# Kernel optimization log

Measured on AMD Instinct MI355X. Metric: run time of the kernel, lower is better.

## Reference

```python
import jax, jax.numpy as jnp
import numpy as np

B, N_RX, IMG_H, IMG_W = 128, 34, 512, 512
N_CAT = 5  # num_rx_categories + 1


def setup_inputs() -> dict:
    key = jax.random.key(0)
    k_pow, k_xy, k_cat, k_dw, k_db, k_cw, k_cb = jax.random.split(key, 7)
    # x_vecs columns: [power, x_coord, y_coord, category]
    powers = jax.random.normal(k_pow, (B, N_RX, 1), dtype=jnp.float32)
    coords = jax.random.randint(k_xy, (B, N_RX, 2), 0, IMG_W).astype(jnp.float32)
    cats = jax.random.randint(k_cat, (B, N_RX, 1), 0, N_CAT).astype(jnp.float32)
    x_vecs = jnp.concatenate([powers, coords, cats], axis=-1)  # [B, N_RX, 4]
    # learned per-device and per-category affine parameters (init: ones/zeros,
    # perturbed slightly so the test is non-trivial)
    device_weights = 1.0 + 0.1 * jax.random.normal(k_dw, (N_RX,), dtype=jnp.float32)
    device_bias = 0.1 * jax.random.normal(k_db, (N_RX,), dtype=jnp.float32)
    category_weights = 1.0 + 0.1 * jax.random.normal(k_cw, (N_CAT,), dtype=jnp.float32)
    category_bias = 0.1 * jax.random.normal(k_cb, (N_CAT,), dtype=jnp.float32)
    return {
        "x_vecs": x_vecs,
        "device_weights": device_weights,
        "device_bias": device_bias,
        "category_weights": category_weights,
        "category_bias": category_bias,
    }


def reference(x_vecs, device_weights, device_bias, category_weights, category_bias):
    batch, n_rx = x_vecs.shape[0], x_vecs.shape[1]
    raw_powers = x_vecs[:, :, 0]                      # [B, N]
    power_mask = (raw_powers != 0).astype(x_vecs.dtype)
    # per-device affine (device_multiplication)
    p = raw_powers * device_weights + power_mask * device_bias
    # per-category affine (category_multiplication)
    cat = x_vecs[:, :, -1].astype(jnp.int32)          # [B, N]
    p = p * category_weights[cat] + power_mask * category_bias[cat]
    # coordinate-based scatter into image grid
    coords = jnp.round(x_vecs[:, :, 1:3]).astype(jnp.int32)  # [B, N, 2] (x, y)
    b_idx = jnp.repeat(jnp.arange(batch), n_rx)
    yy = coords[:, :, 1].ravel()
    xx = coords[:, :, 0].ravel()
    x_img = jnp.zeros((batch, 2, IMG_H, IMG_W), dtype=x_vecs.dtype)
    x_img = x_img.at[b_idx, 0, yy, xx].set(p.ravel())
    x_img = x_img.at[b_idx, 1, yy, xx].set(raw_powers.ravel())
    return x_img
```

## Files before the change

kernel.cpp:

```cpp
#include <hip/hip_runtime.h>

#define B_BATCH 128
#define N_RX 34
#define IMG 512
#define N_CAT 5

__global__ void Vec2Im_scatter_kernel(const float* __restrict__ x_vecs,
                                      const float* __restrict__ device_weights,
                                      const float* __restrict__ device_bias,
                                      const float* __restrict__ category_weights,
                                      const float* __restrict__ category_bias,
                                      float* __restrict__ out) {
    int b = blockIdx.x * blockDim.x + threadIdx.x;
    if (b >= B_BATCH) return;

    const float4* xv = reinterpret_cast<const float4*>(x_vecs) + (size_t)b * N_RX;
    float* plane0 = out + (size_t)b * 2 * IMG * IMG;
    float* plane1 = plane0 + (size_t)IMG * IMG;

    for (int r = 0; r < N_RX; ++r) {
        float4 v = xv[r];
        float raw = v.x;
        float mask = (raw != 0.0f) ? 1.0f : 0.0f;
        float p = raw * device_weights[r] + mask * device_bias[r];
        int cat = (int)v.w;
        p = p * category_weights[cat] + mask * category_bias[cat];
        int xx = (int)rintf(v.y);
        int yy = (int)rintf(v.z);
        int off = yy * IMG + xx;
        plane0[off] = p;
        plane1[off] = raw;
    }
}

extern "C" void kernel_launch(void* const* d_in, const int* in_sizes, int n_in,
                              void* d_out, int out_size, void* d_ws, size_t ws_size,
                              hipStream_t stream) {
    const float* x_vecs           = (const float*)d_in[0];
    const float* device_weights   = (const float*)d_in[1];
    const float* device_bias      = (const float*)d_in[2];
    const float* category_weights = (const float*)d_in[3];
    const float* category_bias    = (const float*)d_in[4];
    float* out = (float*)d_out;

    hipMemsetAsync(d_out, 0, (size_t)out_size * sizeof(float), stream);

    Vec2Im_scatter_kernel<<<1, 128, 0, stream>>>(
        x_vecs, device_weights, device_bias, category_weights, category_bias, out);
}
```

Measured before the change: 275.7 us.

## Fuse zero-fill and scatter into one tiled nontemporal write kernel

Replaces the separate memset plus single-block scatter with one kernel where each block owns a chunk of the output image. Each block computes the transformed entries, filters those falling in its chunk, and writes zeros or values with vectorised nontemporal stores. This removes the second pass over output and the launch of a serial scatter, at the cost of redundant per-block entry computation and a serial filter loop on one thread.

```diff
diff --git a/kernel.cpp b/kernel.cpp
--- a/kernel.cpp
+++ b/kernel.cpp
@@ -3,48 +3,96 @@
 #define B_BATCH 128
 #define N_RX 34
 #define IMG 512
-#define N_CAT 5
+#define PLANE (IMG * IMG)
+#define REGION (2 * PLANE)
+#define THREADS 256
+#define FLOATS_PER_THREAD 16
+#define FLOATS_PER_BLOCK (THREADS * FLOATS_PER_THREAD)
+#define BLOCKS_PER_BATCH (REGION / FLOATS_PER_BLOCK)
+#define N_ENT (2 * N_RX)
 
-__global__ void Vec2Im_scatter_kernel(const float* __restrict__ x_vecs,
-                                      const float* __restrict__ device_weights,
-                                      const float* __restrict__ device_bias,
-                                      const float* __restrict__ category_weights,
-                                      const float* __restrict__ category_bias,
-                                      float* __restrict__ out) {
-    int b = blockIdx.x * blockDim.x + threadIdx.x;
-    if (b >= B_BATCH) return;
+typedef float vfloat4 __attribute__((ext_vector_type(4)));
 
-    const float4* xv = reinterpret_cast<const float4*>(x_vecs) + (size_t)b * N_RX;
-    float* plane0 = out + (size_t)b * 2 * IMG * IMG;
-    float* plane1 = plane0 + (size_t)IMG * IMG;
+__global__ __launch_bounds__(THREADS)
+void Vec2Im_fused_kernel(const float4* __restrict__ xv,
+                         const float* __restrict__ dw,
+                         const float* __restrict__ db,
+                         const float* __restrict__ cw,
+                         const float* __restrict__ cb,
+                         float* __restrict__ out) {
+    __shared__ int   s_pos[N_ENT];
+    __shared__ float s_val[N_ENT];
+    __shared__ int   s_fpos[N_ENT];
+    __shared__ float s_fval[N_ENT];
+    __shared__ int   s_cnt;
 
-    for (int r = 0; r < N_RX; ++r) {
-        float4 v = xv[r];
-        float raw = v.x;
+    const int b     = blockIdx.x >> 7;
+    const int chunk = blockIdx.x & (BLOCKS_PER_BATCH - 1);
+    const int t     = threadIdx.x;
+
+    if (t < N_RX) {
+        float4 v = xv[(size_t)b * N_RX + t];
+        float raw  = v.x;
         float mask = (raw != 0.0f) ? 1.0f : 0.0f;
-        float p = raw * device_weights[r] + mask * device_bias[r];
+        float p = raw * dw[t] + mask * db[t];
         int cat = (int)v.w;
-        p = p * category_weights[cat] + mask * category_bias[cat];
+        p = p * cw[cat] + mask * cb[cat];
         int xx = (int)rintf(v.y);
         int yy = (int)rintf(v.z);
         int off = yy * IMG + xx;
-        plane0[off] = p;
-        plane1[off] = raw;
+        s_pos[t]        = off;               s_val[t]        = p;
+        s_pos[N_RX + t] = off + PLANE;       s_val[N_RX + t] = raw;
     }
+    __syncthreads();
+
+    if (t == 0) {
+        const int lo = chunk * FLOATS_PER_BLOCK;
+        const int hi = lo + FLOATS_PER_BLOCK;
+        int c = 0;
+        for (int i = 0; i < N_ENT; ++i) {
+            int p = s_pos[i];
+            if (p >= lo && p < hi) { s_fpos[c] = p - lo; s_fval[c] = s_val[i]; ++c; }
+        }
+        s_cnt = c;
+    }
+    __syncthreads();
+
+    vfloat4 v0 = {0.f, 0.f, 0.f, 0.f};
+    vfloat4 v1 = {0.f, 0.f, 0.f, 0.f};
+    vfloat4 v2 = {0.f, 0.f, 0.f, 0.f};
+    vfloat4 v3 = {0.f, 0.f, 0.f, 0.f};
+
+    const int cnt = s_cnt;
+    for (int i = 0; i < cnt; ++i) {
+        int q  = s_fpos[i];
+        int f  = q >> 2;
+        bool mine = ((f & (THREADS - 1)) == t);
+        float vv  = s_fval[i];
+        int k  = f >> 8;
+        int e  = q & 3;
+        if (mine && k == 0) { if (e==0) v0.x=vv; else if (e==1) v0.y=vv; else if (e==2) v0.z=vv; else v0.w=vv; }
+        if (mine && k == 1) { if (e==0) v1.x=vv; else if (e==1) v1.y=vv; else if (e==2) v1.z=vv; else v1.w=vv; }
+        if (mine && k == 2) { if (e==0) v2.x=vv; else if (e==1) v2.y=vv; else if (e==2) v2.z=vv; else v2.w=vv; }
+        if (mine && k == 3) { if (e==0) v3.x=vv; else if (e==1) v3.y=vv; else if (e==2) v3.z=vv; else v3.w=vv; }
+    }
+
+    vfloat4* o4 = (vfloat4*)(out + (size_t)b * REGION + (size_t)chunk * FLOATS_PER_BLOCK);
+    __builtin_nontemporal_store(v0, o4 + t);
+    __builtin_nontemporal_store(v1, o4 + THREADS + t);
+    __builtin_nontemporal_store(v2, o4 + 2 * THREADS + t);
+    __builtin_nontemporal_store(v3, o4 + 3 * THREADS + t);
 }
 
 extern "C" void kernel_launch(void* const* d_in, const int* in_sizes, int n_in,
                               void* d_out, int out_size, void* d_ws, size_t ws_size,
                               hipStream_t stream) {
-    const float* x_vecs           = (const float*)d_in[0];
+    const float4* x_vecs          = (const float4*)d_in[0];
     const float* device_weights   = (const float*)d_in[1];
     const float* device_bias      = (const float*)d_in[2];
     const float* category_weights = (const float*)d_in[3];
     const float* category_bias    = (const float*)d_in[4];
     float* out = (float*)d_out;
 
-    hipMemsetAsync(d_out, 0, (size_t)out_size * sizeof(float), stream);
-
-    Vec2Im_scatter_kernel<<<1, 128, 0, stream>>>(
+    Vec2Im_fused_kernel<<<B_BATCH * BLOCKS_PER_BATCH, THREADS, 0, stream>>>(
         x_vecs, device_weights, device_bias, category_weights, category_bias, out);
 }
```

Measured after the change: 288.6 us. +4.7%, slower.
